# Optimization experiments

Measured on AMD Instinct MI355X. Metric: run time of the kernel, lower is better.

The kernel has to match this reference:

```python
import math
import jax, jax.numpy as jnp
import numpy as np


def get_slopes(n):
    def pow2(n):
        start = 2.0 ** (-(2.0 ** (-(math.log2(n) - 3))))
        return [start * (start ** i) for i in range(n)]
    if math.log2(n).is_integer():
        return pow2(n)
    c = 2 ** math.floor(math.log2(n))
    return pow2(c) + get_slopes(2 * c)[0::2][: n - c]


def setup_inputs() -> dict:
    key = jax.random.key(0)
    B, T, C = 2, 2048, 1024
    ks = jax.random.split(key, 9)
    std = 0.02
    n_layers = 12
    inp = {
        "x": jax.random.normal(ks[0], (B, T, C), dtype=jnp.float32),
        # weights stored as [in, out] (transpose of torch Linear.weight)
        "Wq": std * jax.random.normal(ks[1], (C, C), dtype=jnp.float32),
        "bq": jnp.zeros((C,), dtype=jnp.float32),
        "Wk": std * jax.random.normal(ks[2], (C, C), dtype=jnp.float32),
        "bk": jnp.zeros((C,), dtype=jnp.float32),
        "Wv": std * jax.random.normal(ks[3], (C, C), dtype=jnp.float32),
        "bv": jnp.zeros((C,), dtype=jnp.float32),
        # fc_resid gets std 0.02/sqrt(2*num_layers)
        "Wo": (std / math.sqrt(2 * n_layers)) * jax.random.normal(ks[4], (C, C), dtype=jnp.float32),
        "bo": jnp.zeros((C,), dtype=jnp.float32),
        "n_head": 16,
    }
    return inp


def reference(x, Wq, bq, Wk, bk, Wv, bv, Wo, bo, n_head):
    B, T, C = x.shape
    hd = C // n_head
    # QKV projections, split heads: [B, nh, T, hd]
    def proj(W, b):
        return (x @ W + b).reshape(B, T, n_head, hd).transpose(0, 2, 1, 3)
    q, k, v = proj(Wq, bq), proj(Wk, bk), proj(Wv, bv)

    # ALiBi bias: bias[h, i, j] = -slope_h * (i - j) for j <= i, -inf above diag
    slopes = jnp.asarray(get_slopes(n_head), dtype=x.dtype)  # [nh]
    idx = jnp.arange(T)
    dist = (idx[:, None] - idx[None, :]).astype(x.dtype)  # [T, T], i - j
    bias = -slopes[:, None, None] * dist  # [nh, T, T]
    causal = idx[:, None] >= idx[None, :]
    bias = jnp.where(causal[None], bias, jnp.asarray(-jnp.inf, dtype=x.dtype))

    scale = 1.0 / math.sqrt(hd)
    scores = jnp.einsum("bnqh,bnkh->bnqk", q, k) * scale + bias[None]
    att = jax.nn.softmax(scores, axis=-1)
    y = jnp.einsum("bnqk,bnkh->bnqh", att, v)  # [B, nh, T, hd]
    y = y.transpose(0, 2, 1, 3).reshape(B, T, C)
    return y @ Wo + bo
```

## Files before the change

kernel.cpp:

```cpp
#include <hip/hip_runtime.h>


typedef unsigned short u16;
typedef unsigned int u32;
typedef __attribute__((ext_vector_type(8))) short bf16x8;
typedef __attribute__((ext_vector_type(4))) float f32x4;
typedef __attribute__((ext_vector_type(4))) unsigned short u16x4;

#define MFMA16x16(A, B, C_) __builtin_amdgcn_mfma_f32_16x16x32_bf16((A), (B), (C_), 0, 0, 0)

__device__ __forceinline__ u16 f2bf(float f) {
  u32 x = __builtin_bit_cast(u32, f);
  x += 0x7fff + ((x >> 16) & 1);
  return (u16)(x >> 16);
}

__device__ __forceinline__ void gload_lds16(const u16* g, u16* l) {
  __builtin_amdgcn_global_load_lds(
      (const __attribute__((address_space(1))) void*)g,
      (__attribute__((address_space(3))) void*)l, 16, 0, 0);
}

constexpr int T = 2048, C = 1024, HD = 64;
constexpr int BT = 2 * T;

__device__ __forceinline__ bf16x8 ldsfrag(const u16* lds, int row, int kchunk) {
  return *(const bf16x8*)(lds + row * 64 + (((kchunk) ^ (row & 7)) << 3));
}

__global__ __launch_bounds__(256) void prep_kernel(
    const float* __restrict__ xin, u16* __restrict__ xc,
    const float* __restrict__ w0, const float* __restrict__ w1,
    const float* __restrict__ w2, const float* __restrict__ w3,
    u16* __restrict__ wqkvT, u16* __restrict__ woT) {
  __shared__ u16 tile[32][33];
  const int bz = blockIdx.x, tid = threadIdx.x;
  if (bz < 2048) {
    int i = (bz * 256 + tid) * 8;
    const float4 a = *(const float4*)(xin + i);
    const float4 b = *(const float4*)(xin + i + 4);
    uint4 o;
    o.x = (u32)f2bf(a.x) | ((u32)f2bf(a.y) << 16);
    o.y = (u32)f2bf(a.z) | ((u32)f2bf(a.w) << 16);
    o.z = (u32)f2bf(b.x) | ((u32)f2bf(b.y) << 16);
    o.w = (u32)f2bf(b.z) | ((u32)f2bf(b.w) << 16);
    *(uint4*)(xc + i) = o;
    return;
  }
  const int t = bz - 2048;
  const int z = t >> 10, rem = t & 1023;
  const int bx = rem & 31, by = rem >> 5;
  const float* in = (z == 0) ? w0 : (z == 1) ? w1 : (z == 2) ? w2 : w3;
  u16* out = (z < 3) ? (wqkvT + (size_t)z * (1u << 20)) : woT;
  const int tx = tid & 31, ty = tid >> 5;
  int x = bx * 32 + tx;
#pragma unroll
  for (int i = 0; i < 4; i++) {
    int y = by * 32 + ty + i * 8;
    tile[ty + i * 8][tx] = f2bf(in[y * 1024 + x]);
  }
  __syncthreads();
  int xo = by * 32 + tx;
#pragma unroll
  for (int i = 0; i < 4; i++) {
    int yo = bx * 32 + ty + i * 8;
    out[yo * 1024 + xo] = tile[tx][ty + i * 8];
  }
}

__global__ __launch_bounds__(512, 2) void gemm_qkv_kernel(
    const u16* __restrict__ A, const u16* __restrict__ Bt,
    const float* __restrict__ b0, const float* __restrict__ b1,
    const float* __restrict__ b2,
    u16* __restrict__ qout, u16* __restrict__ kout, u16* __restrict__ vtout) {
  constexpr int K = 1024, BK = 32, NT = K / BK;
  __shared__ __align__(16) u16 ring[4][2][256 * BK];

  const int tid = threadIdx.x;
  const int w = tid >> 6, lane = tid & 63;
  const int l15 = lane & 15, quad = lane >> 4;
  const int wr = w >> 2, wc = w & 3;
  const int bid = blockIdx.y * 12 + blockIdx.x;
  const int swz = (bid & 7) * 24 + (bid >> 3);
  const int m0 = (swz / 12) * 256, n0 = (swz % 12) * 256;
  const int rw = lane >> 2;
  const int pc = lane & 3;

  const u16* Ag = A + (size_t)m0 * K;
  const u16* Bg = Bt + (size_t)n0 * K;

  f32x4 acc[8][4] = {};

  auto STAGE = [&](int kt, int s) {
#pragma unroll
    for (int j = 0; j < 2; j++) {
      int row = j * 128 + w * 16 + rw;
      int cl = pc ^ (row & 3);
      gload_lds16(Ag + (size_t)row * K + kt * BK + cl * 8,
                  &ring[s][0][(j * 128 + w * 16) * BK]);
      gload_lds16(Bg + (size_t)row * K + kt * BK + cl * 8,
                  &ring[s][1][(j * 128 + w * 16) * BK]);
    }
  };

  STAGE(0, 0); STAGE(1, 1); STAGE(2, 2);
  asm volatile("s_waitcnt vmcnt(8)" ::: "memory");
  __builtin_amdgcn_s_barrier();

#pragma unroll 1
  for (int t = 0; t < NT; ++t) {
    const int s = t & 3;
    if (t + 3 < NT) STAGE(t + 3, (t + 3) & 3);

    const u16* As = ring[s][0];
    const u16* Bs = ring[s][1];
    bf16x8 bfr[4], afr[8];
#pragma unroll
    for (int ni = 0; ni < 4; ni++) {
      int row = wc * 64 + ni * 16 + l15;
      bfr[ni] = *(const bf16x8*)(Bs + row * BK + ((quad ^ (row & 3)) << 3));
    }
#pragma unroll
    for (int mi = 0; mi < 8; mi++) {
      int row = wr * 128 + mi * 16 + l15;
      afr[mi] = *(const bf16x8*)(As + row * BK + ((quad ^ (row & 3)) << 3));
    }
    __builtin_amdgcn_s_setprio(1);
#pragma unroll
    for (int mi = 0; mi < 8; mi++)
#pragma unroll
      for (int ni = 0; ni < 4; ni++)
        acc[mi][ni] = MFMA16x16(afr[mi], bfr[ni], acc[mi][ni]);
    __builtin_amdgcn_s_setprio(0);

    if (t + 3 < NT)
      asm volatile("s_waitcnt vmcnt(8)" ::: "memory");
    else if (t + 2 < NT)
      asm volatile("s_waitcnt vmcnt(4)" ::: "memory");
    else if (t + 1 < NT)
      asm volatile("s_waitcnt vmcnt(0)" ::: "memory");
    if (t + 1 < NT) __builtin_amdgcn_s_barrier();
  }

  const int sel = n0 >> 10;
  const int nloc = n0 & 1023;
  if (sel < 2) {
    u16* D = (sel == 0) ? qout : kout;
    const float* bias = (sel == 0) ? b0 : b1;
#pragma unroll
    for (int mi = 0; mi < 8; mi++)
#pragma unroll
      for (int ni = 0; ni < 4; ni++) {
        int rb = m0 + wr * 128 + mi * 16 + quad * 4;
        int col = nloc + wc * 64 + ni * 16 + l15;
        float bb = bias[col];
#pragma unroll
        for (int r = 0; r < 4; r++)
          D[(size_t)(rb + r) * 1024 + col] = f2bf(acc[mi][ni][r] + bb);
      }
  } else {
#pragma unroll
    for (int mi = 0; mi < 8; mi++)
#pragma unroll
      for (int ni = 0; ni < 4; ni++) {
        int rb = m0 + wr * 128 + mi * 16 + quad * 4;
        int c = nloc + wc * 64 + ni * 16 + l15;
        float bb = b2[c];
        u16x4 pk;
#pragma unroll
        for (int r = 0; r < 4; r++) pk[r] = f2bf(acc[mi][ni][r] + bb);
        *(u16x4*)(vtout + (size_t)c * 4096 + rb) = pk;
      }
  }
}

__global__ __launch_bounds__(256, 2) void gemm_out_kernel(
    const u16* __restrict__ A, const u16* __restrict__ Bt,
    const float* __restrict__ bias, float* __restrict__ fout) {
  constexpr int K = 1024, BK = 32, NT = K / BK;
  __shared__ __align__(16) u16 ring[4][2][128 * BK];

  const int tid = threadIdx.x;
  const int w = tid >> 6, lane = tid & 63;
  const int l15 = lane & 15, quad = lane >> 4;
  const int wr = w >> 1, wc = w & 1;
  const int bid = blockIdx.y * 8 + blockIdx.x;
  const int swz = (bid & 7) * 32 + (bid >> 3);
  const int m0 = (swz >> 3) * 128, n0 = (swz & 7) * 128;
  const int rw = lane >> 2;
  const int pc = lane & 3;

  const u16* Ag = A + (size_t)m0 * K;
  const u16* Bg = Bt + (size_t)n0 * K;

  f32x4 acc[4][4] = {};

  auto STAGE = [&](int kt, int s) {
#pragma unroll
    for (int j = 0; j < 2; j++) {
      int row = j * 64 + w * 16 + rw;
      int cl = pc ^ (row & 3);
      gload_lds16(Ag + (size_t)row * K + kt * BK + cl * 8,
                  &ring[s][0][(j * 64 + w * 16) * BK]);
      gload_lds16(Bg + (size_t)row * K + kt * BK + cl * 8,
                  &ring[s][1][(j * 64 + w * 16) * BK]);
    }
  };

  STAGE(0, 0); STAGE(1, 1); STAGE(2, 2);
  asm volatile("s_waitcnt vmcnt(8)" ::: "memory");
  __builtin_amdgcn_s_barrier();

#pragma unroll 1
  for (int t = 0; t < NT; ++t) {
    const int s = t & 3;
    if (t + 3 < NT) STAGE(t + 3, (t + 3) & 3);

    const u16* As = ring[s][0];
    const u16* Bs = ring[s][1];
    bf16x8 bfr[4], afr[4];
#pragma unroll
    for (int ni = 0; ni < 4; ni++) {
      int row = wc * 64 + ni * 16 + l15;
      bfr[ni] = *(const bf16x8*)(Bs + row * BK + ((quad ^ (row & 3)) << 3));
    }
#pragma unroll
    for (int mi = 0; mi < 4; mi++) {
      int row = wr * 64 + mi * 16 + l15;
      afr[mi] = *(const bf16x8*)(As + row * BK + ((quad ^ (row & 3)) << 3));
    }
    __builtin_amdgcn_s_setprio(1);
#pragma unroll
    for (int mi = 0; mi < 4; mi++)
#pragma unroll
      for (int ni = 0; ni < 4; ni++)
        acc[mi][ni] = MFMA16x16(afr[mi], bfr[ni], acc[mi][ni]);
    __builtin_amdgcn_s_setprio(0);

    if (t + 3 < NT)
      asm volatile("s_waitcnt vmcnt(8)" ::: "memory");
    else if (t + 2 < NT)
      asm volatile("s_waitcnt vmcnt(4)" ::: "memory");
    else if (t + 1 < NT)
      asm volatile("s_waitcnt vmcnt(0)" ::: "memory");
    if (t + 1 < NT) __builtin_amdgcn_s_barrier();
  }

#pragma unroll
  for (int mi = 0; mi < 4; mi++)
#pragma unroll
    for (int ni = 0; ni < 4; ni++) {
      int rb = m0 + wr * 64 + mi * 16 + quad * 4;
      int col = n0 + wc * 64 + ni * 16 + l15;
      float bb = bias[col];
#pragma unroll
      for (int r = 0; r < 4; r++)
        fout[(size_t)(rb + r) * 1024 + col] = acc[mi][ni][r] + bb;
    }
}

__global__ __launch_bounds__(256, 3) void attn_kernel(
    const u16* __restrict__ qbuf, const u16* __restrict__ kbuf,
    const u16* __restrict__ vtbuf, u16* __restrict__ ybuf) {
  __shared__ __align__(16) u16 KVs[4][64 * 64];
  __shared__ __align__(16) u16 Ps[4][32 * 64];

  const int tid = threadIdx.x;
  const int w = tid >> 6, lane = tid & 63;
  const int wq = w & 1, g = w >> 1;
  const int l15 = lane & 15, quad = lane >> 4;
  const int bh = blockIdx.y, b = bh >> 4, h = bh & 15;
  constexpr float LOG2E = 1.44269504f;
  constexpr float SC = 0.125f * LOG2E;
  const float slope2 = exp2f(-0.5f * (float)(h + 1)) * LOG2E;
  const float slope128 = slope2 * 128.f;
  const float s16 = slope2 * 16.f;
  const int gsub = (lane & 7) ^ ((lane >> 3) & 7);
  const int rsub = lane >> 3;

  const u16* kbase0 = kbuf + (size_t)b * T * C + h * HD;
  const u16* vtbase0 = vtbuf + (size_t)h * HD * BT + (size_t)b * T;
  u16* Pw = Ps[w];
  const int skind = w >> 1;
  const int sjt = w & 1;

#pragma unroll 1
  for (int half = 0; half < 2; half++) {
    const int qt = half == 0 ? (31 - (int)blockIdx.x) : (int)blockIdx.x;

    const u16* qb0 = qbuf + (size_t)(b * T + qt * 64 + wq * 32 + l15) * C + h * HD;
    const u16* qb1 = qb0 + (size_t)16 * C;
    bf16x8 aq00 = *(const bf16x8*)(qb0 + quad * 8);
    bf16x8 aq01 = *(const bf16x8*)(qb0 + 32 + quad * 8);
    bf16x8 aq10 = *(const bf16x8*)(qb1 + quad * 8);
    bf16x8 aq11 = *(const bf16x8*)(qb1 + 32 + quad * 8);

    f32x4 o0[4] = {}, o1[4] = {};
    float lsum0[4] = {0.f, 0.f, 0.f, 0.f};
    float lsum1[4] = {0.f, 0.f, 0.f, 0.f};
    float br[4][4];
    const int ig0 = qt * 64 + wq * 32 + quad * 4;
#pragma unroll
    for (int ni = 0; ni < 4; ni++)
#pragma unroll
      for (int r = 0; r < 4; r++)
        br[ni][r] = slope2 * (float)(g * 64 + ni * 16 + l15 - ig0 - r);

    const int iters = (qt + 2) >> 1;
#pragma unroll 1
    for (int it = 0; it < iters; it++) {
      __syncthreads();
      {
        int jtv = 2 * it + sjt;
        int jtr = jtv > qt ? qt : jtv;
        const u16* base = skind ? (vtbase0 + jtr * 64)
                                : (kbase0 + (size_t)jtr * 64 * C);
        const int stride = skind ? BT : C;
        u16* dst = KVs[w];
#pragma unroll
        for (int c2 = 0; c2 < 8; c2++)
          gload_lds16(base + (size_t)(c2 * 8 + rsub) * stride + gsub * 8,
                      dst + c2 * 8 * 64);
      }
      __syncthreads();

      const int jtv = 2 * it + g;
      const u16* Kw = KVs[g];
      const u16* Vw = KVs[2 + g];

      f32x4 s0[4], s1[4];
#pragma unroll
      for (int ni = 0; ni < 4; ni++) {
        bf16x8 kf0 = ldsfrag(Kw, ni * 16 + l15, quad);
        bf16x8 kf1 = ldsfrag(Kw, ni * 16 + l15, 4 + quad);
        f32x4 z0 = {0.f, 0.f, 0.f, 0.f};
        f32x4 z1 = {0.f, 0.f, 0.f, 0.f};
        z0 = MFMA16x16(aq00, kf0, z0);
        z0 = MFMA16x16(aq01, kf1, z0);
        z1 = MFMA16x16(aq10, kf0, z1);
        z1 = MFMA16x16(aq11, kf1, z1);
        s0[ni] = z0; s1[ni] = z1;
      }

      const bool edge = (jtv >= qt);
#pragma unroll
      for (int ni = 0; ni < 4; ni++)
#pragma unroll
        for (int r = 0; r < 4; r++) {
          const int jj = jtv * 64 + ni * 16 + l15;
          float p0 = exp2f(fmaf(s0[ni][r], SC, br[ni][r]));
          float p1 = exp2f(fmaf(s1[ni][r], SC, br[ni][r]) - s16);
          if (edge) {
            if (jj > ig0 + r) p0 = 0.f;
            if (jj > ig0 + 16 + r) p1 = 0.f;
          }
          lsum0[r] += p0;
          lsum1[r] += p1;
          const int pcol = ni * 16 + l15;
          const int prow0 = quad * 4 + r;
          const int po = (((pcol >> 3) ^ (prow0 & 7)) << 3) + (pcol & 7);
          Pw[prow0 * 64 + po] = f2bf(p0);
          Pw[(prow0 + 16) * 64 + po] = f2bf(p1);
          br[ni][r] += slope128;
        }

      bf16x8 pa00 = ldsfrag(Pw, l15, quad);
      bf16x8 pa01 = ldsfrag(Pw, l15, 4 + quad);
      bf16x8 pa10 = ldsfrag(Pw, 16 + l15, quad);
      bf16x8 pa11 = ldsfrag(Pw, 16 + l15, 4 + quad);
#pragma unroll
      for (int ni = 0; ni < 4; ni++) {
        bf16x8 vf0 = ldsfrag(Vw, ni * 16 + l15, quad);
        bf16x8 vf1 = ldsfrag(Vw, ni * 16 + l15, 4 + quad);
        o0[ni] = MFMA16x16(pa00, vf0, o0[ni]);
        o0[ni] = MFMA16x16(pa01, vf1, o0[ni]);
        o1[ni] = MFMA16x16(pa10, vf0, o1[ni]);
        o1[ni] = MFMA16x16(pa11, vf1, o1[ni]);
      }
    }

    __syncthreads();
    float* sc = (float*)KVs;
    float* Osc = sc + wq * 2048;
    float* Lsc = sc + 4096 + wq * 512;
    if (g == 1) {
#pragma unroll
      for (int ni = 0; ni < 4; ni++)
#pragma unroll
        for (int r = 0; r < 4; r++) {
          Osc[(quad * 4 + r) * 64 + ni * 16 + l15] = o0[ni][r];
          Osc[(16 + quad * 4 + r) * 64 + ni * 16 + l15] = o1[ni][r];
        }
#pragma unroll
      for (int r = 0; r < 4; r++) {
        Lsc[(quad * 4 + r) * 16 + l15] = lsum0[r];
        Lsc[(16 + quad * 4 + r) * 16 + l15] = lsum1[r];
      }
    }
    __syncthreads();
    if (g == 0) {
#pragma unroll
      for (int ni = 0; ni < 4; ni++)
#pragma unroll
        for (int r = 0; r < 4; r++) {
          o0[ni][r] += Osc[(quad * 4 + r) * 64 + ni * 16 + l15];
          o1[ni][r] += Osc[(16 + quad * 4 + r) * 64 + ni * 16 + l15];
        }
#pragma unroll
      for (int r = 0; r < 4; r++) {
        float l0 = lsum0[r] + Lsc[(quad * 4 + r) * 16 + l15];
        float l1 = lsum1[r] + Lsc[(16 + quad * 4 + r) * 16 + l15];
        l0 += __shfl_xor(l0, 1);
        l0 += __shfl_xor(l0, 2);
        l0 += __shfl_xor(l0, 4);
        l0 += __shfl_xor(l0, 8);
        l1 += __shfl_xor(l1, 1);
        l1 += __shfl_xor(l1, 2);
        l1 += __shfl_xor(l1, 4);
        l1 += __shfl_xor(l1, 8);
        float inv0 = 1.f / l0, inv1 = 1.f / l1;
        int row0 = b * T + qt * 64 + wq * 32 + quad * 4 + r;
        u16* y0 = ybuf + (size_t)row0 * C + h * HD;
        u16* y1 = y0 + (size_t)16 * C;
#pragma unroll
        for (int ni = 0; ni < 4; ni++) {
          y0[ni * 16 + l15] = f2bf(o0[ni][r] * inv0);
          y1[ni * 16 + l15] = f2bf(o1[ni][r] * inv1);
        }
      }
    }
  }
}

extern "C" void kernel_launch(void* const* d_in, const int* in_sizes, int n_in,
                              void* d_out, int out_size, void* d_ws, size_t ws_size,
                              hipStream_t stream) {
  (void)in_sizes; (void)n_in; (void)out_size; (void)ws_size;
  const float* x  = (const float*)d_in[0];
  const float* Wq = (const float*)d_in[1];
  const float* bq = (const float*)d_in[2];
  const float* Wk = (const float*)d_in[3];
  const float* bk = (const float*)d_in[4];
  const float* Wv = (const float*)d_in[5];
  const float* bv = (const float*)d_in[6];
  const float* Wo = (const float*)d_in[7];
  const float* bo = (const float*)d_in[8];

  u16* ws = (u16*)d_ws;
  constexpr size_t M1 = 1u << 20;
  u16* wqkvT = ws;
  u16* woT   = ws + 3 * M1;
  u16* xc    = ws + 4 * M1;
  u16* qbuf  = ws + 8 * M1;
  u16* vtbuf = ws + 12 * M1;
  u16* kbuf  = (u16*)d_out;
  u16* ybuf  = qbuf;

  prep_kernel<<<6144, 256, 0, stream>>>(x, xc, Wq, Wk, Wv, Wo, wqkvT, woT);
  gemm_qkv_kernel<<<dim3(12, 16), 512, 0, stream>>>(
      xc, wqkvT, bq, bk, bv, qbuf, kbuf, vtbuf);
  attn_kernel<<<dim3(16, 32), 256, 0, stream>>>(qbuf, kbuf, vtbuf, ybuf);
  gemm_out_kernel<<<dim3(8, 32), 256, 0, stream>>>(ybuf, woT, bo, (float*)d_out);
}
```

Before: 216.0 us.

## Use 128-row query blocks with 8 waves sharing K/V tiles in attention

Restructures the attention kernel so each 512-thread block handles a 128-row query block, with 8 waves sharing each loaded pair of K/V tiles. This replaces the old scheme of 64-row blocks that processed two mirrored query tiles for causal load balancing. Sharing tiles across more query rows is meant to cut K/V global loads per query. Heavier blocks are now launched first, the grid is reordered to head-major, and the exp2 with prescaled constants is replaced by __expf with the plain 0.125 scale. The trade-off is that the mirrored pairing no longer balances causal work across blocks, so the tail of the grid may be uneven.

```diff
diff --git a/kernel.cpp b/kernel.cpp
--- a/kernel.cpp
+++ b/kernel.cpp
@@ -259,174 +259,172 @@
     }
 }
 
-__global__ __launch_bounds__(256, 3) void attn_kernel(
+__global__ __launch_bounds__(512, 4) void attn_kernel(
     const u16* __restrict__ qbuf, const u16* __restrict__ kbuf,
     const u16* __restrict__ vtbuf, u16* __restrict__ ybuf) {
   __shared__ __align__(16) u16 KVs[4][64 * 64];
-  __shared__ __align__(16) u16 Ps[4][32 * 64];
+  __shared__ __align__(16) u16 Ps[8][32 * 64];
 
   const int tid = threadIdx.x;
   const int w = tid >> 6, lane = tid & 63;
-  const int wq = w & 1, g = w >> 1;
+  const int wq = w & 3, g = w >> 2;
   const int l15 = lane & 15, quad = lane >> 4;
-  const int bh = blockIdx.y, b = bh >> 4, h = bh & 15;
-  constexpr float LOG2E = 1.44269504f;
-  constexpr float SC = 0.125f * LOG2E;
-  const float slope2 = exp2f(-0.5f * (float)(h + 1)) * LOG2E;
-  const float slope128 = slope2 * 128.f;
-  const float s16 = slope2 * 16.f;
+  const int bh = blockIdx.x, b = bh >> 4, h = bh & 15;
+  const int qb = 15 - (int)blockIdx.y;
+  const float slope = exp2f(-0.5f * (float)(h + 1));
+  const float slope128 = slope * 128.f;
+  const float s16 = slope * 16.f;
   const int gsub = (lane & 7) ^ ((lane >> 3) & 7);
   const int rsub = lane >> 3;
 
   const u16* kbase0 = kbuf + (size_t)b * T * C + h * HD;
   const u16* vtbase0 = vtbuf + (size_t)h * HD * BT + (size_t)b * T;
   u16* Pw = Ps[w];
-  const int skind = w >> 1;
-  const int sjt = w & 1;
-
+  const int st = w >> 1;
+  const int skind = st & 1;
+  const int sjt = st >> 1;
+  const int srb = (w & 1) * 32;
+
+  const int qt_w = 2 * qb + (wq >> 1);
+  const int row0 = qb * 128 + wq * 32;
+
+  const u16* qp0 = qbuf + (size_t)(b * T + row0 + l15) * C + h * HD;
+  const u16* qp1 = qp0 + (size_t)16 * C;
+  bf16x8 aq00 = *(const bf16x8*)(qp0 + quad * 8);
+  bf16x8 aq01 = *(const bf16x8*)(qp0 + 32 + quad * 8);
+  bf16x8 aq10 = *(const bf16x8*)(qp1 + quad * 8);
+  bf16x8 aq11 = *(const bf16x8*)(qp1 + 32 + quad * 8);
+
+  f32x4 o0[4] = {}, o1[4] = {};
+  float lsum0[4] = {0.f, 0.f, 0.f, 0.f};
+  float lsum1[4] = {0.f, 0.f, 0.f, 0.f};
+  float br[4][4];
+  const int ig0 = row0 + quad * 4;
+#pragma unroll
+  for (int ni = 0; ni < 4; ni++)
+#pragma unroll
+    for (int r = 0; r < 4; r++)
+      br[ni][r] = slope * (float)(g * 64 + ni * 16 + l15 - ig0 - r);
+
+  const int iters = qb + 1;
 #pragma unroll 1
-  for (int half = 0; half < 2; half++) {
-    const int qt = half == 0 ? (31 - (int)blockIdx.x) : (int)blockIdx.x;
-
-    const u16* qb0 = qbuf + (size_t)(b * T + qt * 64 + wq * 32 + l15) * C + h * HD;
-    const u16* qb1 = qb0 + (size_t)16 * C;
-    bf16x8 aq00 = *(const bf16x8*)(qb0 + quad * 8);
-    bf16x8 aq01 = *(const bf16x8*)(qb0 + 32 + quad * 8);
-    bf16x8 aq10 = *(const bf16x8*)(qb1 + quad * 8);
-    bf16x8 aq11 = *(const bf16x8*)(qb1 + 32 + quad * 8);
-
-    f32x4 o0[4] = {}, o1[4] = {};
-    float lsum0[4] = {0.f, 0.f, 0.f, 0.f};
-    float lsum1[4] = {0.f, 0.f, 0.f, 0.f};
-    float br[4][4];
-    const int ig0 = qt * 64 + wq * 32 + quad * 4;
+  for (int it = 0; it < iters; it++) {
+    __syncthreads();
+    {
+      const int jtv = 2 * it + sjt;
+      const u16* base = skind ? (vtbase0 + jtv * 64)
+                              : (kbase0 + (size_t)jtv * 64 * C);
+      const int stride = skind ? BT : C;
+      u16* dst = KVs[skind * 2 + sjt] + srb * 64;
+#pragma unroll
+      for (int c2 = 0; c2 < 4; c2++)
+        gload_lds16(base + (size_t)(srb + c2 * 8 + rsub) * stride + gsub * 8,
+                    dst + c2 * 8 * 64);
+    }
+    __syncthreads();
+
+    const int jtv = 2 * it + g;
+    const u16* Kw = KVs[g];
+    const u16* Vw = KVs[2 + g];
+
+    f32x4 s0[4], s1[4];
+#pragma unroll
+    for (int ni = 0; ni < 4; ni++) {
+      bf16x8 kf0 = ldsfrag(Kw, ni * 16 + l15, quad);
+      bf16x8 kf1 = ldsfrag(Kw, ni * 16 + l15, 4 + quad);
+      f32x4 z0 = {0.f, 0.f, 0.f, 0.f};
+      f32x4 z1 = {0.f, 0.f, 0.f, 0.f};
+      z0 = MFMA16x16(aq00, kf0, z0);
+      z0 = MFMA16x16(aq01, kf1, z0);
+      z1 = MFMA16x16(aq10, kf0, z1);
+      z1 = MFMA16x16(aq11, kf1, z1);
+      s0[ni] = z0; s1[ni] = z1;
+    }
+
+    const bool edge = (jtv >= qt_w);
 #pragma unroll
     for (int ni = 0; ni < 4; ni++)
 #pragma unroll
-      for (int r = 0; r < 4; r++)
-        br[ni][r] = slope2 * (float)(g * 64 + ni * 16 + l15 - ig0 - r);
-
-    const int iters = (qt + 2) >> 1;
-#pragma unroll 1
-    for (int it = 0; it < iters; it++) {
-      __syncthreads();
-      {
-        int jtv = 2 * it + sjt;
-        int jtr = jtv > qt ? qt : jtv;
-        const u16* base = skind ? (vtbase0 + jtr * 64)
-                                : (kbase0 + (size_t)jtr * 64 * C);
-        const int stride = skind ? BT : C;
-        u16* dst = KVs[w];
-#pragma unroll
-        for (int c2 = 0; c2 < 8; c2++)
-          gload_lds16(base + (size_t)(c2 * 8 + rsub) * stride + gsub * 8,
-                      dst + c2 * 8 * 64);
-      }
-      __syncthreads();
-
-      const int jtv = 2 * it + g;
-      const u16* Kw = KVs[g];
-      const u16* Vw = KVs[2 + g];
-
-      f32x4 s0[4], s1[4];
+      for (int r = 0; r < 4; r++) {
+        const int jj = jtv * 64 + ni * 16 + l15;
+        float p0 = __expf(fmaf(s0[ni][r], 0.125f, br[ni][r]));
+        float p1 = __expf(fmaf(s1[ni][r], 0.125f, br[ni][r]) - s16);
+        if (edge) {
+          if (jj > ig0 + r) p0 = 0.f;
+          if (jj > ig0 + 16 + r) p1 = 0.f;
+        }
+        lsum0[r] += p0;
+        lsum1[r] += p1;
+        const int pcol = ni * 16 + l15;
+        const int prow = quad * 4 + r;
+        const int po = (((pcol >> 3) ^ (prow & 7)) << 3) + (pcol & 7);
+        Pw[prow * 64 + po] = f2bf(p0);
+        Pw[(prow + 16) * 64 + po] = f2bf(p1);
+        br[ni][r] += slope128;
+      }
+
+    bf16x8 pa00 = ldsfrag(Pw, l15, quad);
+    bf16x8 pa01 = ldsfrag(Pw, l15, 4 + quad);
+    bf16x8 pa10 = ldsfrag(Pw, 16 + l15, quad);
+    bf16x8 pa11 = ldsfrag(Pw, 16 + l15, 4 + quad);
+#pragma unroll
+    for (int ni = 0; ni < 4; ni++) {
+      bf16x8 vf0 = ldsfrag(Vw, ni * 16 + l15, quad);
+      bf16x8 vf1 = ldsfrag(Vw, ni * 16 + l15, 4 + quad);
+      o0[ni] = MFMA16x16(pa00, vf0, o0[ni]);
+      o0[ni] = MFMA16x16(pa01, vf1, o0[ni]);
+      o1[ni] = MFMA16x16(pa10, vf0, o1[ni]);
+      o1[ni] = MFMA16x16(pa11, vf1, o1[ni]);
+    }
+  }
+
+  __syncthreads();
+  float* Osc = (float*)KVs;
+  float* Lsc = (float*)Ps;
+  const int rb0 = wq * 32 + quad * 4;
+  if (g == 1) {
+#pragma unroll
+    for (int ni = 0; ni < 4; ni++)
+#pragma unroll
+      for (int r = 0; r < 4; r++) {
+        Osc[(rb0 + r) * 64 + ni * 16 + l15] = o0[ni][r];
+        Osc[(rb0 + 16 + r) * 64 + ni * 16 + l15] = o1[ni][r];
+      }
+#pragma unroll
+    for (int r = 0; r < 4; r++) {
+      Lsc[(rb0 + r) * 16 + l15] = lsum0[r];
+      Lsc[(rb0 + 16 + r) * 16 + l15] = lsum1[r];
+    }
+  }
+  __syncthreads();
+  if (g == 0) {
+#pragma unroll
+    for (int ni = 0; ni < 4; ni++)
+#pragma unroll
+      for (int r = 0; r < 4; r++) {
+        o0[ni][r] += Osc[(rb0 + r) * 64 + ni * 16 + l15];
+        o1[ni][r] += Osc[(rb0 + 16 + r) * 64 + ni * 16 + l15];
+      }
+#pragma unroll
+    for (int r = 0; r < 4; r++) {
+      float l0 = lsum0[r] + Lsc[(rb0 + r) * 16 + l15];
+      float l1 = lsum1[r] + Lsc[(rb0 + 16 + r) * 16 + l15];
+      l0 += __shfl_xor(l0, 1);
+      l0 += __shfl_xor(l0, 2);
+      l0 += __shfl_xor(l0, 4);
+      l0 += __shfl_xor(l0, 8);
+      l1 += __shfl_xor(l1, 1);
+      l1 += __shfl_xor(l1, 2);
+      l1 += __shfl_xor(l1, 4);
+      l1 += __shfl_xor(l1, 8);
+      float inv0 = 1.f / l0, inv1 = 1.f / l1;
+      int row_g = b * T + qb * 128 + rb0 + r;
+      u16* y0 = ybuf + (size_t)row_g * C + h * HD;
+      u16* y1 = y0 + (size_t)16 * C;
 #pragma unroll
       for (int ni = 0; ni < 4; ni++) {
-        bf16x8 kf0 = ldsfrag(Kw, ni * 16 + l15, quad);
-        bf16x8 kf1 = ldsfrag(Kw, ni * 16 + l15, 4 + quad);
-        f32x4 z0 = {0.f, 0.f, 0.f, 0.f};
-        f32x4 z1 = {0.f, 0.f, 0.f, 0.f};
-        z0 = MFMA16x16(aq00, kf0, z0);
-        z0 = MFMA16x16(aq01, kf1, z0);
-        z1 = MFMA16x16(aq10, kf0, z1);
-        z1 = MFMA16x16(aq11, kf1, z1);
-        s0[ni] = z0; s1[ni] = z1;
-      }
-
-      const bool edge = (jtv >= qt);
-#pragma unroll
-      for (int ni = 0; ni < 4; ni++)
-#pragma unroll
-        for (int r = 0; r < 4; r++) {
-          const int jj = jtv * 64 + ni * 16 + l15;
-          float p0 = exp2f(fmaf(s0[ni][r], SC, br[ni][r]));
-          float p1 = exp2f(fmaf(s1[ni][r], SC, br[ni][r]) - s16);
-          if (edge) {
-            if (jj > ig0 + r) p0 = 0.f;
-            if (jj > ig0 + 16 + r) p1 = 0.f;
-          }
-          lsum0[r] += p0;
-          lsum1[r] += p1;
-          const int pcol = ni * 16 + l15;
-          const int prow0 = quad * 4 + r;
-          const int po = (((pcol >> 3) ^ (prow0 & 7)) << 3) + (pcol & 7);
-          Pw[prow0 * 64 + po] = f2bf(p0);
-          Pw[(prow0 + 16) * 64 + po] = f2bf(p1);
-          br[ni][r] += slope128;
-        }
-
-      bf16x8 pa00 = ldsfrag(Pw, l15, quad);
-      bf16x8 pa01 = ldsfrag(Pw, l15, 4 + quad);
-      bf16x8 pa10 = ldsfrag(Pw, 16 + l15, quad);
-      bf16x8 pa11 = ldsfrag(Pw, 16 + l15, 4 + quad);
-#pragma unroll
-      for (int ni = 0; ni < 4; ni++) {
-        bf16x8 vf0 = ldsfrag(Vw, ni * 16 + l15, quad);
-        bf16x8 vf1 = ldsfrag(Vw, ni * 16 + l15, 4 + quad);
-        o0[ni] = MFMA16x16(pa00, vf0, o0[ni]);
-        o0[ni] = MFMA16x16(pa01, vf1, o0[ni]);
-        o1[ni] = MFMA16x16(pa10, vf0, o1[ni]);
-        o1[ni] = MFMA16x16(pa11, vf1, o1[ni]);
-      }
-    }
-
-    __syncthreads();
-    float* sc = (float*)KVs;
-    float* Osc = sc + wq * 2048;
-    float* Lsc = sc + 4096 + wq * 512;
-    if (g == 1) {
-#pragma unroll
-      for (int ni = 0; ni < 4; ni++)
-#pragma unroll
-        for (int r = 0; r < 4; r++) {
-          Osc[(quad * 4 + r) * 64 + ni * 16 + l15] = o0[ni][r];
-          Osc[(16 + quad * 4 + r) * 64 + ni * 16 + l15] = o1[ni][r];
-        }
-#pragma unroll
-      for (int r = 0; r < 4; r++) {
-        Lsc[(quad * 4 + r) * 16 + l15] = lsum0[r];
-        Lsc[(16 + quad * 4 + r) * 16 + l15] = lsum1[r];
-      }
-    }
-    __syncthreads();
-    if (g == 0) {
-#pragma unroll
-      for (int ni = 0; ni < 4; ni++)
-#pragma unroll
-        for (int r = 0; r < 4; r++) {
-          o0[ni][r] += Osc[(quad * 4 + r) * 64 + ni * 16 + l15];
-          o1[ni][r] += Osc[(16 + quad * 4 + r) * 64 + ni * 16 + l15];
-        }
-#pragma unroll
-      for (int r = 0; r < 4; r++) {
-        float l0 = lsum0[r] + Lsc[(quad * 4 + r) * 16 + l15];
-        float l1 = lsum1[r] + Lsc[(16 + quad * 4 + r) * 16 + l15];
-        l0 += __shfl_xor(l0, 1);
-        l0 += __shfl_xor(l0, 2);
-        l0 += __shfl_xor(l0, 4);
-        l0 += __shfl_xor(l0, 8);
-        l1 += __shfl_xor(l1, 1);
-        l1 += __shfl_xor(l1, 2);
-        l1 += __shfl_xor(l1, 4);
-        l1 += __shfl_xor(l1, 8);
-        float inv0 = 1.f / l0, inv1 = 1.f / l1;
-        int row0 = b * T + qt * 64 + wq * 32 + quad * 4 + r;
-        u16* y0 = ybuf + (size_t)row0 * C + h * HD;
-        u16* y1 = y0 + (size_t)16 * C;
-#pragma unroll
-        for (int ni = 0; ni < 4; ni++) {
-          y0[ni * 16 + l15] = f2bf(o0[ni][r] * inv0);
-          y1[ni * 16 + l15] = f2bf(o1[ni][r] * inv1);
-        }
+        y0[ni * 16 + l15] = f2bf(o0[ni][r] * inv0);
+        y1[ni * 16 + l15] = f2bf(o1[ni][r] * inv1);
       }
     }
   }
@@ -459,6 +457,6 @@
   prep_kernel<<<6144, 256, 0, stream>>>(x, xc, Wq, Wk, Wv, Wo, wqkvT, woT);
   gemm_qkv_kernel<<<dim3(12, 16), 512, 0, stream>>>(
       xc, wqkvT, bq, bk, bv, qbuf, kbuf, vtbuf);
-  attn_kernel<<<dim3(16, 32), 256, 0, stream>>>(qbuf, kbuf, vtbuf, ybuf);
+  attn_kernel<<<dim3(32, 16), 512, 0, stream>>>(qbuf, kbuf, vtbuf, ybuf);
   gemm_out_kernel<<<dim3(8, 32), 256, 0, stream>>>(ybuf, woT, bo, (float*)d_out);
 }
```

New measurement: 237.1 us. +9.8%, slower.
